# Performance work log

Measured on AMD Instinct MI355X. Metric: run time of the kernel, lower is better.

The kernel has to match this reference:

```python
import jax, jax.numpy as jnp
import numpy as np

N = 10000
E = 160000
F_IN = 64
HID = 128
HEADS = 8
NC = 3
NEG_SLOPE = 0.2
EPS = 1e-16


def setup_inputs() -> dict:
    key = jax.random.key(0)
    ks = jax.random.split(key, 12)
    p = lambda k, shape: jax.random.normal(k, shape, jnp.float32) * 0.1
    return {
        "x": jax.random.normal(ks[0], (N, F_IN), jnp.float32),
        "edge_index": jax.random.randint(ks[1], (2, E), 0, N),
        # conv1: F_IN -> 8 heads x 128, concat -> 1024
        "W1": p(ks[2], (F_IN, HEADS * HID)),
        "a_src1": p(ks[3], (HEADS, HID)),
        "a_dst1": p(ks[4], (HEADS, HID)),
        "b1": jnp.zeros((HEADS * HID,), jnp.float32),
        # conv2: 1024 -> 8 heads x 64, concat -> 512
        "W2": p(ks[5], (HEADS * HID, HEADS * (HID // 2))),
        "a_src2": p(ks[6], (HEADS, HID // 2)),
        "a_dst2": p(ks[7], (HEADS, HID // 2)),
        "b2": jnp.zeros((HEADS * (HID // 2),), jnp.float32),
        # conv3: 512 -> 1 head x 3, mean (concat=False)
        "W3": p(ks[8], (HEADS * (HID // 2), NC)),
        "a_src3": p(ks[9], (1, NC)),
        "a_dst3": p(ks[10], (1, NC)),
        "b3": jnp.zeros((NC,), jnp.float32),
    }


def gat_conv(x, src, dst, W, a_src, a_dst, b, concat):
    """PyG-style GATConv (eval mode, self-loops already in src/dst)."""
    n = x.shape[0]
    H, C = a_src.shape
    h = (x @ W).reshape(n, H, C)                      # [N, H, C]
    s_src = jnp.sum(h * a_src[None], axis=-1)         # [N, H]
    s_dst = jnp.sum(h * a_dst[None], axis=-1)         # [N, H]
    e = jax.nn.leaky_relu(s_src[src] + s_dst[dst], NEG_SLOPE)  # [E, H]
    # segment softmax over incoming edges per destination node
    m = jax.ops.segment_max(e, dst, num_segments=n)   # [N, H]
    ex = jnp.exp(e - m[dst])
    denom = jax.ops.segment_sum(ex, dst, num_segments=n)
    alpha = ex / (denom[dst] + EPS)                   # [E, H]
    msg = h[src] * alpha[:, :, None]                  # [E, H, C]
    out = jax.ops.segment_sum(msg, dst, num_segments=n)  # [N, H, C]
    out = out.reshape(n, H * C) if concat else out.mean(axis=1)
    return out + b


def reference(x, edge_index, W1, a_src1, a_dst1, b1, W2, a_src2, a_dst2, b2, W3, a_src3, a_dst3, b3):
    n = x.shape[0]
    loop = jnp.arange(n, dtype=edge_index.dtype)
    src = jnp.concatenate([edge_index[0], loop])
    dst = jnp.concatenate([edge_index[1], loop])
    h = gat_conv(x, src, dst, W1, a_src1, a_dst1, b1, True)
    h = jax.nn.elu(h)
    h = gat_conv(h, src, dst, W2, a_src2, a_dst2, b2, True)
    h = jax.nn.elu(h)
    h = gat_conv(h, src, dst, W3, a_src3, a_dst3, b3, False)
    return jax.nn.log_softmax(h, axis=1)
```

## Files before the change

### kernel.cpp

```cpp
#include <hip/hip_runtime.h>
#include <math.h>

#define NEG_SLOPE 0.2f
#define EPS_DEN 1e-16f

typedef __attribute__((ext_vector_type(8))) short bf16x8;
typedef __attribute__((ext_vector_type(4))) float f32x4;

__device__ inline void split2(float a, short& hi, short& lo) {
    unsigned u = __float_as_uint(a);
    unsigned uh = (u + 0x8000u) & 0xFFFF0000u;
    float fh = __uint_as_float(uh);
    hi = (short)(uh >> 16);
    float r = a - fh;
    lo = (short)((__float_as_uint(r) + 0x8000u) >> 16);
}

__device__ inline unsigned short f2bf(float f) {
    unsigned u = __float_as_uint(f);
    return (unsigned short)((u + 0x7FFFu + ((u >> 16) & 1u)) >> 16);
}
__device__ inline float bflo(unsigned u) { return __uint_as_float(u << 16); }
__device__ inline float bfhi(unsigned u) { return __uint_as_float(u & 0xFFFF0000u); }

__global__ void k_count(const int* __restrict__ ei, int E, int Nn, int* counts) {
    int e = blockIdx.x * blockDim.x + threadIdx.x;
    int ET = E + Nn;
    if (e >= ET) return;
    int d = (e < E) ? ei[E + e] : (e - E);
    atomicAdd(&counts[d], 1);
}

__global__ void k_scan(const int* __restrict__ counts, int Nn, int ET, int* __restrict__ row_off) {
    __shared__ int lds[256];
    int t = threadIdx.x;
    int chunk = (Nn + 255) / 256;
    int b0 = t * chunk, b1 = min(Nn, b0 + chunk);
    int s = 0;
    for (int i = b0; i < b1; i++) s += counts[i];
    lds[t] = s;
    __syncthreads();
    if (t == 0) {
        int run = 0;
        for (int i = 0; i < 256; i++) { int v = lds[i]; lds[i] = run; run += v; }
    }
    __syncthreads();
    int run = lds[t];
    for (int i = b0; i < b1; i++) { row_off[i] = run; run += counts[i]; }
    if (t == 0) row_off[Nn] = ET;
}

__global__ void k_scatter(const int* __restrict__ ei, int E, int Nn,
                          const int* __restrict__ row_off, int* cursor, int* __restrict__ col) {
    int e = blockIdx.x * blockDim.x + threadIdx.x;
    int ET = E + Nn;
    if (e >= ET) return;
    int d = (e < E) ? ei[E + e] : (e - E);
    int s = (e < E) ? ei[e] : (e - E);
    int pos = atomicAdd(&cursor[d], 1);
    col[row_off[d] + pos] = s;
}

__global__ void k_split_x(const float* __restrict__ x, short* __restrict__ A,
                          int M, int Mp, int K) {
    int i = blockIdx.x * blockDim.x + threadIdx.x;
    if (i >= Mp * K) return;
    int row = i / K, c = i - row * K;
    float v = (row < M) ? x[(size_t)row * K + c] : 0.f;
    short hi, lo;
    split2(v, hi, lo);
    A[(size_t)row * (2 * K) + c] = hi;
    A[(size_t)row * (2 * K) + K + c] = lo;
}

__global__ __launch_bounds__(256) void k_split_wt(const float* __restrict__ W,
                                                  short* __restrict__ Bt, int K, int N, int dup) {
    __shared__ float s[32][33];
    int k0 = blockIdx.x * 32, n0 = blockIdx.y * 32;
    int tx = threadIdx.x & 31, ty = threadIdx.x >> 5;
    for (int r = ty; r < 32; r += 8) s[r][tx] = W[(size_t)(k0 + r) * N + n0 + tx];
    __syncthreads();
    int ldbt = (1 + dup) * K;
    for (int r = ty; r < 32; r += 8) {
        float v = s[tx][r];
        unsigned u = __float_as_uint(v);
        short hi = (short)((u + 0x7FFFu + ((u >> 16) & 1u)) >> 16);
        size_t base = (size_t)(n0 + r) * ldbt + k0 + tx;
        Bt[base] = hi;
        if (dup) Bt[base + K] = hi;
    }
}

__global__ __launch_bounds__(256) void k_mfma64(const short* __restrict__ A,
                                                const short* __restrict__ B,
                                                unsigned short* __restrict__ C,
                                                int M, int N, int Ktot,
                                                int lda, int ldb) {
    __shared__ short As[64 * 32];
    __shared__ short Bs[64 * 32];
    int t = threadIdx.x;
    int lane = t & 63;
    int wid = t >> 6;

    int nbx = N >> 6;
    int nb = gridDim.x;
    int q = nb >> 3, r = nb & 7;
    int xcd = blockIdx.x & 7, pos = blockIdx.x >> 3;
    int L = (xcd < r ? xcd * (q + 1) : r * (q + 1) + (xcd - r) * q) + pos;
    int bn = (L % nbx) * 64;
    int bm = (L / nbx) * 64;

    int wm = (wid >> 1) * 32, wn = (wid & 1) * 32;
    int fr = lane & 15, kq = lane >> 4;

    int srow = t >> 2, sslot = t & 3;
    int sko = ((sslot ^ ((srow >> 1) & 3)) << 3);

    f32x4 acc[2][2] = {};

    for (int k0 = 0; k0 < Ktot; k0 += 32) {
        {
            const short* sa = A + (size_t)(bm + srow) * lda + k0 + sko;
            const short* sb = B + (size_t)(bn + srow) * ldb + k0 + sko;
            short* da = As + (size_t)(wid << 6) * 8;
            short* db = Bs + (size_t)(wid << 6) * 8;
            __builtin_amdgcn_global_load_lds((const __attribute__((address_space(1))) void*)sa,
                                             (__attribute__((address_space(3))) void*)da, 16, 0, 0);
            __builtin_amdgcn_global_load_lds((const __attribute__((address_space(1))) void*)sb,
                                             (__attribute__((address_space(3))) void*)db, 16, 0, 0);
        }
        __syncthreads();
        bf16x8 af[2], bfv[2];
        #pragma unroll
        for (int i = 0; i < 2; i++) {
            int rowa = wm + i * 16 + fr;
            int rowb = wn + i * 16 + fr;
            af[i]  = *(const bf16x8*)(As + rowa * 32 + ((kq ^ ((rowa >> 1) & 3)) << 3));
            bfv[i] = *(const bf16x8*)(Bs + rowb * 32 + ((kq ^ ((rowb >> 1) & 3)) << 3));
        }
        #pragma unroll
        for (int i = 0; i < 2; i++)
            #pragma unroll
            for (int j = 0; j < 2; j++)
                acc[i][j] = __builtin_amdgcn_mfma_f32_16x16x32_bf16(af[i], bfv[j], acc[i][j], 0, 0, 0);
        __syncthreads();
    }
    #pragma unroll
    for (int i = 0; i < 2; i++) {
        int rbase = bm + wm + i * 16 + kq * 4;
        #pragma unroll
        for (int j = 0; j < 2; j++) {
            int colc = bn + wn + j * 16 + fr;
            #pragma unroll
            for (int rg = 0; rg < 4; rg++) {
                int rr = rbase + rg;
                if (rr < M) C[(size_t)rr * N + colc] = f2bf(acc[i][j][rg]);
            }
        }
    }
}

template<int H, int C>
__global__ __launch_bounds__(256) void k_scores_bf(const unsigned short* __restrict__ h,
                                                   const float* __restrict__ a_src,
                                                   const float* __restrict__ a_dst,
                                                   float* __restrict__ ssrc,
                                                   float* __restrict__ sdst, int Nn) {
    constexpr int D = H * C;
    constexpr int PER = D / 64;
    constexpr int GRP = C / PER;
    int lane = threadIdx.x & 63;
    int n = blockIdx.x * 4 + (threadIdx.x >> 6);
    if (n >= Nn) return;
    const unsigned short* hp = h + (size_t)n * D + lane * PER;
    int cb = lane * PER;
    float as = 0.f, ad = 0.f;
    #pragma unroll
    for (int j0 = 0; j0 < PER; j0 += 8) {
        uint4 u = *(const uint4*)(hp + j0);
        int c = cb + j0;
        as += bflo(u.x) * a_src[c + 0] + bfhi(u.x) * a_src[c + 1]
            + bflo(u.y) * a_src[c + 2] + bfhi(u.y) * a_src[c + 3]
            + bflo(u.z) * a_src[c + 4] + bfhi(u.z) * a_src[c + 5]
            + bflo(u.w) * a_src[c + 6] + bfhi(u.w) * a_src[c + 7];
        ad += bflo(u.x) * a_dst[c + 0] + bfhi(u.x) * a_dst[c + 1]
            + bflo(u.y) * a_dst[c + 2] + bfhi(u.y) * a_dst[c + 3]
            + bflo(u.z) * a_dst[c + 4] + bfhi(u.z) * a_dst[c + 5]
            + bflo(u.w) * a_dst[c + 6] + bfhi(u.w) * a_dst[c + 7];
    }
    #pragma unroll
    for (int off = GRP >> 1; off >= 1; off >>= 1) {
        as += __shfl_xor(as, off);
        ad += __shfl_xor(ad, off);
    }
    if ((lane & (GRP - 1)) == 0) {
        int hh = lane / GRP;
        ssrc[n * H + hh] = as;
        sdst[n * H + hh] = ad;
    }
}

__global__ __launch_bounds__(256) void k_gemm_n3s(const float* __restrict__ A, const float* __restrict__ W,
                                                  const float* __restrict__ as3, const float* __restrict__ ad3,
                                                  float* __restrict__ C3, float* __restrict__ ssrc,
                                                  float* __restrict__ sdst, int M, int K) {
    __shared__ float lw[1536];
    int t = threadIdx.x;
    for (int i = t; i < K * 3; i += 256) lw[i] = W[i];
    __syncthreads();
    int lane = t & 63;
    int n = blockIdx.x * 4 + (t >> 6);
    if (n >= M) return;
    float a0 = 0.f, a1 = 0.f, a2 = 0.f;
    for (int c = lane; c < K; c += 64) {
        float v = A[(size_t)n * K + c];
        a0 += v * lw[c * 3 + 0];
        a1 += v * lw[c * 3 + 1];
        a2 += v * lw[c * 3 + 2];
    }
    #pragma unroll
    for (int off = 32; off > 0; off >>= 1) {
        a0 += __shfl_xor(a0, off);
        a1 += __shfl_xor(a1, off);
        a2 += __shfl_xor(a2, off);
    }
    if (lane == 0) {
        C3[n * 3 + 0] = a0; C3[n * 3 + 1] = a1; C3[n * 3 + 2] = a2;
        ssrc[n] = a0 * as3[0] + a1 * as3[1] + a2 * as3[2];
        sdst[n] = a0 * ad3[0] + a1 * ad3[1] + a2 * ad3[2];
    }
}

template<int H, int C, bool ELU, bool BFOUT>
__global__ __launch_bounds__(256) void k_agg_bf(const unsigned short* __restrict__ hsrc,
                                                const float* __restrict__ ssrc,
                                                const float* __restrict__ sdst,
                                                const int* __restrict__ col,
                                                const int* __restrict__ row_off,
                                                const float* __restrict__ bias,
                                                float* __restrict__ out,
                                                unsigned short* __restrict__ osp) {
    constexpr int D = H * C;
    constexpr int VEC = D / 256;
    int n = blockIdx.x, t = threadIdx.x;
    int head = (VEC * t) / C;
    int beg = row_off[n], end = row_off[n + 1];
    __shared__ int s_col[32];
    __shared__ float s_ex[32 * H];
    __shared__ float sh_sd[H];
    if (t < H) sh_sd[t] = sdst[n * H + t];
    float acc[VEC];
    float den = 0.f;
    #pragma unroll
    for (int v = 0; v < VEC; v++) acc[v] = 0.f;

    for (int j0 = beg; j0 < end; j0 += 32) {
        int nb = min(32, end - j0);
        __syncthreads();
        if (t < nb) s_col[t] = col[j0 + t];
        if (t < nb * H) {
            int e = t >> 3, hh = t & 7;
            int cj = col[j0 + e];
            float s = ssrc[cj * H + hh] + sh_sd[hh];
            s = (s >= 0.f) ? s : NEG_SLOPE * s;
            s_ex[t] = __expf(s);
        }
        __syncthreads();
        for (int i = 0; i < nb; i++) {
            const unsigned short* hp = hsrc + (size_t)s_col[i] * D + VEC * t;
            float a = s_ex[i * H + head];
            den += a;
            if (VEC == 4) {
                uint2 u = *(const uint2*)hp;
                acc[0] += a * bflo(u.x);
                acc[1] += a * bfhi(u.x);
                acc[2] += a * bflo(u.y);
                acc[3] += a * bfhi(u.y);
            } else {
                unsigned u = *(const unsigned*)hp;
                acc[0] += a * bflo(u);
                acc[1] += a * bfhi(u);
            }
        }
    }
    float iv = 1.f / (den + EPS_DEN);
    #pragma unroll
    for (int v = 0; v < VEC; v++) {
        int idx = VEC * t + v;
        float val = acc[v] * iv + bias[idx];
        if (ELU) val = (val > 0.f) ? val : (__expf(val) - 1.f);
        if (BFOUT) osp[(size_t)n * D + idx] = f2bf(val);
        else       out[(size_t)n * D + idx] = val;
    }
}

__global__ void k_l3_fused(const float* __restrict__ h3, const float* __restrict__ ssrc,
                           const float* __restrict__ sdst, const int* __restrict__ col,
                           const int* __restrict__ row_off, const float* __restrict__ b3,
                           float* __restrict__ out, int Nn) {
    int n = blockIdx.x * blockDim.x + threadIdx.x;
    if (n >= Nn) return;
    int beg = row_off[n], end = row_off[n + 1];
    float sd = sdst[n];
    float den = 0.f, a0 = 0.f, a1 = 0.f, a2 = 0.f;
    for (int j = beg; j < end; j++) {
        int sI = col[j];
        float s = ssrc[sI] + sd;
        s = (s >= 0.f) ? s : NEG_SLOPE * s;
        float ex = __expf(s);
        den += ex;
        a0 += ex * h3[sI * 3 + 0];
        a1 += ex * h3[sI * 3 + 1];
        a2 += ex * h3[sI * 3 + 2];
    }
    float iv = 1.f / (den + EPS_DEN);
    float v0 = a0 * iv + b3[0], v1 = a1 * iv + b3[1], v2 = a2 * iv + b3[2];
    float m = fmaxf(v0, fmaxf(v1, v2));
    float l = logf(__expf(v0 - m) + __expf(v1 - m) + __expf(v2 - m));
    out[n * 3 + 0] = v0 - m - l;
    out[n * 3 + 1] = v1 - m - l;
    out[n * 3 + 2] = v2 - m - l;
}

extern "C" void kernel_launch(void* const* d_in, const int* in_sizes, int n_in,
                              void* d_out, int out_size, void* d_ws, size_t ws_size,
                              hipStream_t stream) {
    (void)n_in; (void)out_size; (void)ws_size;
    const float* x   = (const float*)d_in[0];
    const int*   ei  = (const int*)d_in[1];
    const float* W1  = (const float*)d_in[2];
    const float* as1 = (const float*)d_in[3];
    const float* ad1 = (const float*)d_in[4];
    const float* b1  = (const float*)d_in[5];
    const float* W2  = (const float*)d_in[6];
    const float* as2 = (const float*)d_in[7];
    const float* ad2 = (const float*)d_in[8];
    const float* b2  = (const float*)d_in[9];
    const float* W3  = (const float*)d_in[10];
    const float* as3 = (const float*)d_in[11];
    const float* ad3 = (const float*)d_in[12];
    const float* b3  = (const float*)d_in[13];
    float* out = (float*)d_out;

    const int Nn = in_sizes[0] / 64;
    const int E  = in_sizes[1] / 2;
    const int ET = E + Nn;
    const int Mp = ((Nn + 127) / 128) * 128;

    char* ws = (char*)d_ws;
    size_t off = 0;
    auto alloc = [&](size_t bytes) -> void* {
        void* p = ws + off;
        off = (off + bytes + 255) & ~(size_t)255;
        return p;
    };
    unsigned short* hbuf = (unsigned short*)alloc((size_t)Mp * 1024 * 2);
    void*  big  = alloc((size_t)Mp * 1024 * 2 + 65536);
    unsigned short* A2 = (unsigned short*)big;
    float* obuf = (float*)big;
    float* h3   = (float*)alloc((size_t)Nn * 3 * 4);
    short* A1   = (short*)alloc((size_t)Mp * 128 * 2);
    short* B1t  = (short*)alloc((size_t)1024 * 128 * 2);
    short* B2t  = (short*)alloc((size_t)512 * 1024 * 2);
    float* ssrc = (float*)alloc((size_t)Nn * 8 * 4);
    float* sdst = (float*)alloc((size_t)Nn * 8 * 4);
    int* counts = (int*)alloc((size_t)Nn * 2 * 4);
    int* cursor = counts + Nn;
    int* row_off= (int*)alloc((size_t)(Nn + 1) * 4);
    int* colb   = (int*)alloc((size_t)ET * 4);

    hipMemsetAsync(counts, 0, (size_t)Nn * 2 * 4, stream);

    int etb = (ET + 255) / 256;
    k_count<<<etb, 256, 0, stream>>>(ei, E, Nn, counts);
    k_scan<<<1, 256, 0, stream>>>(counts, Nn, ET, row_off);
    k_scatter<<<etb, 256, 0, stream>>>(ei, E, Nn, row_off, cursor, colb);

    k_split_x<<<(Mp * 64 + 255) / 256, 256, 0, stream>>>(x, A1, Nn, Mp, 64);
    k_split_wt<<<dim3(64 / 32, 1024 / 32), 256, 0, stream>>>(W1, B1t, 64, 1024, 1);
    k_split_wt<<<dim3(1024 / 32, 512 / 32), 256, 0, stream>>>(W2, B2t, 1024, 512, 0);

    {
        int nb = (1024 / 64) * (Mp / 64);
        k_mfma64<<<nb, 256, 0, stream>>>(A1, B1t, hbuf, Nn, 1024, 128, 128, 128);
        k_scores_bf<8, 128><<<(Nn + 3) / 4, 256, 0, stream>>>(hbuf, as1, ad1, ssrc, sdst, Nn);
        k_agg_bf<8, 128, true, true><<<Nn, 256, 0, stream>>>(hbuf, ssrc, sdst, colb, row_off, b1, nullptr, A2);
    }
    {
        int nb = (512 / 64) * (Mp / 64);
        k_mfma64<<<nb, 256, 0, stream>>>((const short*)A2, B2t, hbuf, Nn, 512, 1024, 1024, 1024);
        k_scores_bf<8, 64><<<(Nn + 3) / 4, 256, 0, stream>>>(hbuf, as2, ad2, ssrc, sdst, Nn);
        k_agg_bf<8, 64, true, false><<<Nn, 256, 0, stream>>>(hbuf, ssrc, sdst, colb, row_off, b2, obuf, nullptr);
    }
    {
        k_gemm_n3s<<<(Nn + 3) / 4, 256, 0, stream>>>(obuf, W3, as3, ad3, h3, ssrc, sdst, Nn, 512);
        k_l3_fused<<<(Nn + 255) / 256, 256, 0, stream>>>(h3, ssrc, sdst, colb, row_off, b3, out, Nn);
    }
}
```

Before: 198.9 us.

## Rewrite GAT aggregation as wave-per-node kernel with 16-byte gathers

Replaces the block-per-node aggregation, which staged neighbor indices and exp scores in shared memory behind two barriers per chunk, with a kernel where each 64-lane wavefront handles a node or half a node. Each lane computes its own head's attention weight and gathers 8 bf16 values with one 16-byte load. Output is written with vector stores. This removes the shared-memory staging and __syncthreads, at the cost of recomputing each exp once per lane instead of once per block. A leftover unused k_agg_wv template duplicates the new kernel.

```diff
diff --git a/kernel.cpp b/kernel.cpp
--- a/kernel.cpp
+++ b/kernel.cpp
@@ -231,8 +231,8 @@
     }
 }
 
-template<int H, int C, bool ELU, bool BFOUT>
-__global__ __launch_bounds__(256) void k_agg_bf(const unsigned short* __restrict__ hsrc,
+template<int H, int C, int CB, bool ELU, bool BFOUT>
+__global__ __launch_bounds__(256) void k_agg_wv(const unsigned short* __restrict__ hsrc,
                                                 const float* __restrict__ ssrc,
                                                 const float* __restrict__ sdst,
                                                 const int* __restrict__ col,
@@ -241,56 +241,108 @@
                                                 float* __restrict__ out,
                                                 unsigned short* __restrict__ osp) {
     constexpr int D = H * C;
-    constexpr int VEC = D / 256;
-    int n = blockIdx.x, t = threadIdx.x;
-    int head = (VEC * t) / C;
+    int lane = threadIdx.x & 63;
+    int w = blockIdx.x * 4 + (threadIdx.x >> 6);
+    if (w >= 10000 * CB) {}
+    int n, cb;
+    if (CB == 2) { n = w >> 1; cb = w & 1; } else { n = w; cb = 0; }
+    int col0 = cb * 512 + lane * 8;
+    int myhead = col0 / C;
+    float sd = sdst[n * H + myhead];
     int beg = row_off[n], end = row_off[n + 1];
-    __shared__ int s_col[32];
-    __shared__ float s_ex[32 * H];
-    __shared__ float sh_sd[H];
-    if (t < H) sh_sd[t] = sdst[n * H + t];
-    float acc[VEC];
+    const unsigned short* hbase = hsrc + col0;
+
+    float acc[8] = {0.f, 0.f, 0.f, 0.f, 0.f, 0.f, 0.f, 0.f};
     float den = 0.f;
-    #pragma unroll
-    for (int v = 0; v < VEC; v++) acc[v] = 0.f;
-
-    for (int j0 = beg; j0 < end; j0 += 32) {
-        int nb = min(32, end - j0);
-        __syncthreads();
-        if (t < nb) s_col[t] = col[j0 + t];
-        if (t < nb * H) {
-            int e = t >> 3, hh = t & 7;
-            int cj = col[j0 + e];
-            float s = ssrc[cj * H + hh] + sh_sd[hh];
-            s = (s >= 0.f) ? s : NEG_SLOPE * s;
-            s_ex[t] = __expf(s);
-        }
-        __syncthreads();
-        for (int i = 0; i < nb; i++) {
-            const unsigned short* hp = hsrc + (size_t)s_col[i] * D + VEC * t;
-            float a = s_ex[i * H + head];
-            den += a;
-            if (VEC == 4) {
-                uint2 u = *(const uint2*)hp;
-                acc[0] += a * bflo(u.x);
-                acc[1] += a * bfhi(u.x);
-                acc[2] += a * bflo(u.y);
-                acc[3] += a * bfhi(u.y);
-            } else {
-                unsigned u = *(const unsigned*)hp;
-                acc[0] += a * bflo(u);
-                acc[1] += a * bfhi(u);
-            }
-        }
+    #pragma unroll 2
+    for (int j = beg; j < end; j++) {
+        int cj = col[j];
+        float s = ssrc[cj * H + myhead] + sd;
+        s = (s >= 0.f) ? s : NEG_SLOPE * s;
+        float ex = __expf(s);
+        den += ex;
+        uint4 u = *(const uint4*)(hbase + (size_t)cj * D);
+        acc[0] += ex * bflo(u.x); acc[1] += ex * bfhi(u.x);
+        acc[2] += ex * bflo(u.y); acc[3] += ex * bfhi(u.y);
+        acc[4] += ex * bflo(u.z); acc[5] += ex * bfhi(u.z);
+        acc[6] += ex * bflo(u.w); acc[7] += ex * bfhi(u.w);
     }
     float iv = 1.f / (den + EPS_DEN);
-    #pragma unroll
-    for (int v = 0; v < VEC; v++) {
-        int idx = VEC * t + v;
-        float val = acc[v] * iv + bias[idx];
+    float vals[8];
+    #pragma unroll
+    for (int v = 0; v < 8; v++) {
+        float val = acc[v] * iv + bias[col0 + v];
         if (ELU) val = (val > 0.f) ? val : (__expf(val) - 1.f);
-        if (BFOUT) osp[(size_t)n * D + idx] = f2bf(val);
-        else       out[(size_t)n * D + idx] = val;
+        vals[v] = val;
+    }
+    if (BFOUT) {
+        uint4 o;
+        o.x = (unsigned)f2bf(vals[0]) | ((unsigned)f2bf(vals[1]) << 16);
+        o.y = (unsigned)f2bf(vals[2]) | ((unsigned)f2bf(vals[3]) << 16);
+        o.z = (unsigned)f2bf(vals[4]) | ((unsigned)f2bf(vals[5]) << 16);
+        o.w = (unsigned)f2bf(vals[6]) | ((unsigned)f2bf(vals[7]) << 16);
+        *(uint4*)(osp + (size_t)n * D + col0) = o;
+    } else {
+        *(f32x4*)(out + (size_t)n * D + col0) = *(f32x4*)&vals[0];
+        *(f32x4*)(out + (size_t)n * D + col0 + 4) = *(f32x4*)&vals[4];
+    }
+}
+
+template<int H, int C, int CB, bool ELU, bool BFOUT>
+__global__ __launch_bounds__(256) void k_agg_wave(const unsigned short* __restrict__ hsrc,
+                                                  const float* __restrict__ ssrc,
+                                                  const float* __restrict__ sdst,
+                                                  const int* __restrict__ col,
+                                                  const int* __restrict__ row_off,
+                                                  const float* __restrict__ bias,
+                                                  float* __restrict__ out,
+                                                  unsigned short* __restrict__ osp,
+                                                  int nw) {
+    constexpr int D = H * C;
+    int lane = threadIdx.x & 63;
+    int w = blockIdx.x * 4 + (threadIdx.x >> 6);
+    if (w >= nw) return;
+    int n, cb;
+    if (CB == 2) { n = w >> 1; cb = w & 1; } else { n = w; cb = 0; }
+    int col0 = cb * 512 + lane * 8;
+    int myhead = col0 / C;
+    float sd = sdst[n * H + myhead];
+    int beg = row_off[n], end = row_off[n + 1];
+    const unsigned short* hbase = hsrc + col0;
+
+    float acc[8] = {0.f, 0.f, 0.f, 0.f, 0.f, 0.f, 0.f, 0.f};
+    float den = 0.f;
+    #pragma unroll 2
+    for (int j = beg; j < end; j++) {
+        int cj = col[j];
+        float s = ssrc[cj * H + myhead] + sd;
+        s = (s >= 0.f) ? s : NEG_SLOPE * s;
+        float ex = __expf(s);
+        den += ex;
+        uint4 u = *(const uint4*)(hbase + (size_t)cj * D);
+        acc[0] += ex * bflo(u.x); acc[1] += ex * bfhi(u.x);
+        acc[2] += ex * bflo(u.y); acc[3] += ex * bfhi(u.y);
+        acc[4] += ex * bflo(u.z); acc[5] += ex * bfhi(u.z);
+        acc[6] += ex * bflo(u.w); acc[7] += ex * bfhi(u.w);
+    }
+    float iv = 1.f / (den + EPS_DEN);
+    float vals[8];
+    #pragma unroll
+    for (int v = 0; v < 8; v++) {
+        float val = acc[v] * iv + bias[col0 + v];
+        if (ELU) val = (val > 0.f) ? val : (__expf(val) - 1.f);
+        vals[v] = val;
+    }
+    if (BFOUT) {
+        uint4 o;
+        o.x = (unsigned)f2bf(vals[0]) | ((unsigned)f2bf(vals[1]) << 16);
+        o.y = (unsigned)f2bf(vals[2]) | ((unsigned)f2bf(vals[3]) << 16);
+        o.z = (unsigned)f2bf(vals[4]) | ((unsigned)f2bf(vals[5]) << 16);
+        o.w = (unsigned)f2bf(vals[6]) | ((unsigned)f2bf(vals[7]) << 16);
+        *(uint4*)(osp + (size_t)n * D + col0) = o;
+    } else {
+        *(f32x4*)(out + (size_t)n * D + col0) = *(f32x4*)&vals[0];
+        *(f32x4*)(out + (size_t)n * D + col0 + 4) = *(f32x4*)&vals[4];
     }
 }
 
@@ -384,13 +436,15 @@
         int nb = (1024 / 64) * (Mp / 64);
         k_mfma64<<<nb, 256, 0, stream>>>(A1, B1t, hbuf, Nn, 1024, 128, 128, 128);
         k_scores_bf<8, 128><<<(Nn + 3) / 4, 256, 0, stream>>>(hbuf, as1, ad1, ssrc, sdst, Nn);
-        k_agg_bf<8, 128, true, true><<<Nn, 256, 0, stream>>>(hbuf, ssrc, sdst, colb, row_off, b1, nullptr, A2);
+        int nw = Nn * 2;
+        k_agg_wave<8, 128, 2, true, true><<<(nw + 3) / 4, 256, 0, stream>>>(hbuf, ssrc, sdst, colb, row_off, b1, nullptr, A2, nw);
     }
     {
         int nb = (512 / 64) * (Mp / 64);
         k_mfma64<<<nb, 256, 0, stream>>>((const short*)A2, B2t, hbuf, Nn, 512, 1024, 1024, 1024);
         k_scores_bf<8, 64><<<(Nn + 3) / 4, 256, 0, stream>>>(hbuf, as2, ad2, ssrc, sdst, Nn);
-        k_agg_bf<8, 64, true, false><<<Nn, 256, 0, stream>>>(hbuf, ssrc, sdst, colb, row_off, b2, obuf, nullptr);
+        int nw = Nn;
+        k_agg_wave<8, 64, 1, true, false><<<(nw + 3) / 4, 256, 0, stream>>>(hbuf, ssrc, sdst, colb, row_off, b2, obuf, nullptr, nw);
     }
     {
         k_gemm_n3s<<<(Nn + 3) / 4, 256, 0, stream>>>(obuf, W3, as3, ad3, h3, ssrc, sdst, Nn, 512);
```

After: 199.3 us. Within noise of the previous version (+0.2%).
